# Performance work log

Hardware: AMD Instinct MI355X
Metric: run time of the kernel (lower is better)

The kernel has to match this reference:

```python
import jax, jax.numpy as jnp
import numpy as np

BS, Q, K, NT = 16, 1500, 256, 150   # batch, queries, classes, GT per image (T = BS*NT)
COST_CLASS, COST_BBOX, COST_GIOU = 1.0, 5.0, 2.0
ALPHA, GAMMA, EPS = 0.25, 2.0, 1e-8


def box_cxcywh_to_xyxy(b):
    cx, cy, w, h = b[..., 0], b[..., 1], b[..., 2], b[..., 3]
    return jnp.stack([cx - 0.5 * w, cy - 0.5 * h, cx + 0.5 * w, cy + 0.5 * h], axis=-1)


def generalized_box_iou(boxes1, boxes2):
    # boxes in xyxy; boxes1: [N,4], boxes2: [M,4] -> [N,M]
    area1 = (boxes1[:, 2] - boxes1[:, 0]) * (boxes1[:, 3] - boxes1[:, 1])
    area2 = (boxes2[:, 2] - boxes2[:, 0]) * (boxes2[:, 3] - boxes2[:, 1])
    lt = jnp.maximum(boxes1[:, None, :2], boxes2[None, :, :2])
    rb = jnp.minimum(boxes1[:, None, 2:], boxes2[None, :, 2:])
    wh = jnp.clip(rb - lt, 0.0)
    inter = wh[..., 0] * wh[..., 1]
    union = area1[:, None] + area2[None, :] - inter
    iou = inter / union
    # smallest enclosing box
    lt_e = jnp.minimum(boxes1[:, None, :2], boxes2[None, :, :2])
    rb_e = jnp.maximum(boxes1[:, None, 2:], boxes2[None, :, 2:])
    wh_e = jnp.clip(rb_e - lt_e, 0.0)
    area_e = wh_e[..., 0] * wh_e[..., 1]
    return iou - (area_e - union) / area_e


def setup_inputs() -> dict:
    key = jax.random.key(0)
    k1, k2, k3, k4 = jax.random.split(key, 4)
    pred_logits = jax.random.normal(k1, (BS, Q, K), dtype=jnp.float32)
    pred_boxes = jax.random.uniform(k2, (BS, Q, 4), dtype=jnp.float32, minval=0.05, maxval=0.95)
    tgt_bbox = jax.random.uniform(k3, (BS * NT, 4), dtype=jnp.float32, minval=0.05, maxval=0.95)
    tgt_ids = jax.random.randint(k4, (BS * NT,), 0, K)
    return {"pred_logits": pred_logits, "pred_boxes": pred_boxes,
            "tgt_bbox": tgt_bbox, "tgt_ids": tgt_ids}


def reference(pred_logits, pred_boxes, tgt_bbox, tgt_ids):
    bs, nq, k = pred_logits.shape
    out_prob = jax.nn.sigmoid(pred_logits.reshape(bs * nq, k))   # [N, K]
    out_bbox = pred_boxes.reshape(bs * nq, 4)                    # [N, 4]

    # focal-style classification cost, gathered at target class columns
    neg_cost = (1.0 - ALPHA) * out_prob ** GAMMA * -jnp.log(1.0 - out_prob + EPS)
    pos_cost = ALPHA * (1.0 - out_prob) ** GAMMA * -jnp.log(out_prob + EPS)
    cost_class = (pos_cost - neg_cost)[:, tgt_ids]               # [N, T]

    # L1 box cost (cdist p=1)
    cost_bbox = jnp.sum(jnp.abs(out_bbox[:, None, :] - tgt_bbox[None, :, :]), axis=-1)

    # negative GIoU cost
    cost_giou = -generalized_box_iou(box_cxcywh_to_xyxy(out_bbox),
                                     box_cxcywh_to_xyxy(tgt_bbox))

    C = COST_BBOX * cost_bbox + COST_CLASS * cost_class + COST_GIOU * cost_giou
    return C.reshape(bs, nq, -1)                                  # [bs, Q, T]
```

## Files before the change

kernel.cpp:

```cpp
#include <hip/hip_runtime.h>
#include <hip/hip_fp16.h>


namespace {
constexpr int kBS = 16, kQ = 1500, kK = 256, kNT = 150;
constexpr int kT   = kBS * kNT;
constexpr int kN   = kBS * kQ;
constexpr int kQB  = 8;
constexpr float kAlpha = 0.25f;
constexpr float kEps   = 1e-8f;
typedef float floatx4 __attribute__((ext_vector_type(4)));
}

__global__ __launch_bounds__(256, 6)
void matcher_cost_kernel(const float* __restrict__ logits,
                         const float* __restrict__ pboxes,
                         const float* __restrict__ tboxes,
                         const int*   __restrict__ tids,
                         float* __restrict__ out)
{
    __shared__ __align__(16) __half2 s_fcl[kK][6];

    const int tid = threadIdx.x;
    const int n0  = blockIdx.x * kQB;

    {
        const float* lrow = logits + (size_t)n0 * kK + tid;
#pragma unroll
        for (int qp = 0; qp < kQB / 2; ++qp) {
            float c[2];
#pragma unroll
            for (int j = 0; j < 2; ++j) {
                const float x   = lrow[(2 * qp + j) * kK];
                const float p   = __builtin_amdgcn_rcpf(1.0f + __expf(-x));
                const float omp = 1.0f - p;
                c[j] = -kAlpha * omp * omp * __logf(p + kEps)
                     + (1.0f - kAlpha) * p * p * __logf(omp + kEps) + 2.0f;
            }
            s_fcl[tid][qp] = __floats2half2_rn(c[0], c[1]);
        }
    }
    __syncthreads();

    const float4* __restrict__ tb4   = reinterpret_cast<const float4*>(tboxes);
    const char*   __restrict__ fbase = reinterpret_cast<const char*>(s_fcl);

    auto tilework = [&](int tbase) {
        const int4 ci = *reinterpret_cast<const int4*>(tids + tbase);
        const int laddr[4] = {ci.x * 24, ci.y * 24, ci.z * 24, ci.w * 24};
        float4 tb[4];
#pragma unroll
        for (int e = 0; e < 4; ++e) tb[e] = tb4[tbase + e];
        float* __restrict__ ob = out + (size_t)n0 * kT + tbase;

#pragma unroll
        for (int qg = 0; qg < kQB / 4; ++qg) {
            uint2 ccr[4];
#pragma unroll
            for (int e = 0; e < 4; ++e)
                ccr[e] = *reinterpret_cast<const uint2*>(
                             fbase + laddr[e] + qg * 8);

#pragma unroll
            for (int qi = 0; qi < 4; ++qi) {
                const int q = qg * 4 + qi;
                const float4 pb = *reinterpret_cast<const float4*>(
                                      pboxes + (size_t)(n0 + q) * 4);
                const float pcx = pb.x, pcy = pb.y, pw = pb.z, ph = pb.w;
                const float px1 = fmaf(-0.5f, pw, pcx), px2 = fmaf(0.5f, pw, pcx);
                const float py1 = fmaf(-0.5f, ph, pcy), py2 = fmaf(0.5f, ph, pcy);
                const float parea = pw * ph;

                floatx4 res;
#pragma unroll
                for (int e = 0; e < 4; ++e) {
                    const unsigned u  = (qi < 2) ? ccr[e].x : ccr[e].y;
                    const __half2 h2  = *reinterpret_cast<const __half2*>(&u);
                    const float   cc  = (qi & 1) ? __high2float(h2) : __low2float(h2);
                    const float bcx = tb[e].x, bcy = tb[e].y;
                    const float bw  = tb[e].z, bh  = tb[e].w;
                    const float cb = fabsf(pcx - bcx) + fabsf(pcy - bcy)
                                   + fabsf(pw - bw)  + fabsf(ph - bh);
                    const float bx1 = fmaf(-0.5f, bw, bcx), bx2 = fmaf(0.5f, bw, bcx);
                    const float by1 = fmaf(-0.5f, bh, bcy), by2 = fmaf(0.5f, bh, bcy);
                    const float ow = fminf(px2, bx2) - fmaxf(px1, bx1);
                    const float oh = fminf(py2, by2) - fmaxf(py1, by1);
                    const float iw = fmaxf(ow, 0.0f), ih = fmaxf(oh, 0.0f);
                    const float ew = (pw + bw) - ow, eh = (ph + bh) - oh;
                    const float inter = iw * ih;
                    const float uni   = fmaf(bw, bh, parea) - inter;
                    const float ear   = ew * eh;
                    const float rr   = __builtin_amdgcn_rcpf(uni * ear);
                    const float frac = fmaf(uni, uni, inter * ear) * rr;
                    res[e] = fmaf(-2.0f, frac, fmaf(5.0f, cb, cc));
                }
                __builtin_nontemporal_store(
                    res, reinterpret_cast<floatx4*>(ob + (size_t)q * kT));
            }
        }
    };

    const int o4 = tid << 2;
    tilework(o4);
    tilework(1024 + o4);
    if (o4 < 352) tilework(2048 + o4);
}

extern "C" void kernel_launch(void* const* d_in, const int* in_sizes, int n_in,
                              void* d_out, int out_size, void* d_ws, size_t ws_size,
                              hipStream_t stream) {
    const float* logits = (const float*)d_in[0];
    const float* pboxes = (const float*)d_in[1];
    const float* tboxes = (const float*)d_in[2];
    const int*   tids   = (const int*)d_in[3];
    float* out = (float*)d_out;

    dim3 grid(kN / kQB);
    dim3 block(256);
    hipLaunchKernelGGL(matcher_cost_kernel, grid, block, 0, stream,
                       logits, pboxes, tboxes, tids, out);
}
```

Before: 265.0 us.

## Hoist target loads before logits stage and interleave target tiles per query

Target ids and boxes for all three column tiles are now loaded into registers before the sigmoid/focal-cost stage, so their latency overlaps with the logits work. The loop order becomes query-outer, tile-inner, so each query box is loaded once and the three tiles' stores are interleaved. Nontemporal stores are replaced with ordinary float4 stores, and launch bounds drop from 6 to 4 waves per SIMD to allow more registers for the larger live state. This trades occupancy and higher register pressure for better latency hiding and fewer redundant loads.

```diff
diff --git a/kernel.cpp b/kernel.cpp
--- a/kernel.cpp
+++ b/kernel.cpp
@@ -9,10 +9,9 @@
 constexpr int kQB  = 8;
 constexpr float kAlpha = 0.25f;
 constexpr float kEps   = 1e-8f;
-typedef float floatx4 __attribute__((ext_vector_type(4)));
 }
 
-__global__ __launch_bounds__(256, 6)
+__global__ __launch_bounds__(256, 4)
 void matcher_cost_kernel(const float* __restrict__ logits,
                          const float* __restrict__ pboxes,
                          const float* __restrict__ tboxes,
@@ -23,6 +22,24 @@
 
     const int tid = threadIdx.x;
     const int n0  = blockIdx.x * kQB;
+    const int o4  = tid << 2;
+    const bool t2 = o4 < 352;
+
+    const float4* __restrict__ tb4 = reinterpret_cast<const float4*>(tboxes);
+    float4 tb[3][4];
+    int laddr[3][4];
+#pragma unroll
+    for (int t = 0; t < 3; ++t) {
+        const int tbase = t * 1024 + o4;
+        const bool act  = (t < 2) || t2;
+        const int4 ci   = act ? *reinterpret_cast<const int4*>(tids + tbase)
+                              : make_int4(0, 0, 0, 0);
+        laddr[t][0] = ci.x * 24; laddr[t][1] = ci.y * 24;
+        laddr[t][2] = ci.z * 24; laddr[t][3] = ci.w * 24;
+#pragma unroll
+        for (int e = 0; e < 4; ++e)
+            tb[t][e] = act ? tb4[tbase + e] : make_float4(0.f, 0.f, 1.f, 1.f);
+    }
 
     {
         const float* lrow = logits + (size_t)n0 * kK + tid;
@@ -42,43 +59,41 @@
     }
     __syncthreads();
 
-    const float4* __restrict__ tb4   = reinterpret_cast<const float4*>(tboxes);
-    const char*   __restrict__ fbase = reinterpret_cast<const char*>(s_fcl);
-
-    auto tilework = [&](int tbase) {
-        const int4 ci = *reinterpret_cast<const int4*>(tids + tbase);
-        const int laddr[4] = {ci.x * 24, ci.y * 24, ci.z * 24, ci.w * 24};
-        float4 tb[4];
-#pragma unroll
-        for (int e = 0; e < 4; ++e) tb[e] = tb4[tbase + e];
-        float* __restrict__ ob = out + (size_t)n0 * kT + tbase;
+    const char* __restrict__ fbase = reinterpret_cast<const char*>(s_fcl);
+    float* __restrict__ ob = out + (size_t)n0 * kT;
 
 #pragma unroll
-        for (int qg = 0; qg < kQB / 4; ++qg) {
-            uint2 ccr[4];
+    for (int qg = 0; qg < kQB / 4; ++qg) {
+        uint2 ccr[3][4];
+#pragma unroll
+        for (int t = 0; t < 3; ++t)
 #pragma unroll
             for (int e = 0; e < 4; ++e)
-                ccr[e] = *reinterpret_cast<const uint2*>(
-                             fbase + laddr[e] + qg * 8);
+                ccr[t][e] = *reinterpret_cast<const uint2*>(
+                                fbase + laddr[t][e] + qg * 8);
 
 #pragma unroll
-            for (int qi = 0; qi < 4; ++qi) {
-                const int q = qg * 4 + qi;
-                const float4 pb = *reinterpret_cast<const float4*>(
-                                      pboxes + (size_t)(n0 + q) * 4);
-                const float pcx = pb.x, pcy = pb.y, pw = pb.z, ph = pb.w;
-                const float px1 = fmaf(-0.5f, pw, pcx), px2 = fmaf(0.5f, pw, pcx);
-                const float py1 = fmaf(-0.5f, ph, pcy), py2 = fmaf(0.5f, ph, pcy);
-                const float parea = pw * ph;
+        for (int qi = 0; qi < 4; ++qi) {
+            const int q = qg * 4 + qi;
+            const float4 pb = *reinterpret_cast<const float4*>(
+                                  pboxes + (size_t)(n0 + q) * 4);
+            const float pcx = pb.x, pcy = pb.y, pw = pb.z, ph = pb.w;
+            const float px1 = fmaf(-0.5f, pw, pcx), px2 = fmaf(0.5f, pw, pcx);
+            const float py1 = fmaf(-0.5f, ph, pcy), py2 = fmaf(0.5f, ph, pcy);
+            const float parea = pw * ph;
 
-                floatx4 res;
+#pragma unroll
+            for (int t = 0; t < 3; ++t) {
+                if (t == 2 && !t2) continue;
+                float4 res; float* rp = &res.x;
 #pragma unroll
                 for (int e = 0; e < 4; ++e) {
-                    const unsigned u  = (qi < 2) ? ccr[e].x : ccr[e].y;
+                    const unsigned u  = (qi < 2) ? ccr[t][e].x : ccr[t][e].y;
                     const __half2 h2  = *reinterpret_cast<const __half2*>(&u);
-                    const float   cc  = (qi & 1) ? __high2float(h2) : __low2float(h2);
-                    const float bcx = tb[e].x, bcy = tb[e].y;
-                    const float bw  = tb[e].z, bh  = tb[e].w;
+                    const float   cc  = (qi & 1) ? __high2float(h2)
+                                                 : __low2float(h2);
+                    const float bcx = tb[t][e].x, bcy = tb[t][e].y;
+                    const float bw  = tb[t][e].z, bh  = tb[t][e].w;
                     const float cb = fabsf(pcx - bcx) + fabsf(pcy - bcy)
                                    + fabsf(pw - bw)  + fabsf(ph - bh);
                     const float bx1 = fmaf(-0.5f, bw, bcx), bx2 = fmaf(0.5f, bw, bcx);
@@ -92,18 +107,12 @@
                     const float ear   = ew * eh;
                     const float rr   = __builtin_amdgcn_rcpf(uni * ear);
                     const float frac = fmaf(uni, uni, inter * ear) * rr;
-                    res[e] = fmaf(-2.0f, frac, fmaf(5.0f, cb, cc));
+                    rp[e] = fmaf(-2.0f, frac, fmaf(5.0f, cb, cc));
                 }
-                __builtin_nontemporal_store(
-                    res, reinterpret_cast<floatx4*>(ob + (size_t)q * kT));
+                *reinterpret_cast<float4*>(ob + (size_t)q * kT + t * 1024 + o4) = res;
             }
         }
-    };
-
-    const int o4 = tid << 2;
-    tilework(o4);
-    tilework(1024 + o4);
-    if (o4 < 352) tilework(2048 + o4);
+    }
 }
 
 extern "C" void kernel_launch(void* const* d_in, const int* in_sizes, int n_in,
```

After: 374.9 us. 1.41x slower.
